# Kernel optimization log

Hardware: AMD Instinct MI355X
Metric: run time of the kernel (lower is better)

## Reference

```python
import jax, jax.numpy as jnp
import numpy as np

H = 64          # hidden_size / SINDy latent dim
DM = 128        # d_model (GRU input size)
FF = 128        # dim_feedforward
NL = 2          # num_sindy_layers
EPS = 1e-5      # LayerNorm eps (torch default)
TRI_I, TRI_J = np.triu_indices(H)          # poly_order=2 pairs, torch loop order (i<=j)
LIB = 1 + H + TRI_I.size                   # 2145


def layernorm(x, g, b):
    m = jnp.mean(x, axis=-1, keepdims=True)
    v = jnp.mean((x - m) ** 2, axis=-1, keepdims=True)
    return (x - m) * jax.lax.rsqrt(v + EPS) * g + b


def sindy_library(z):
    # z: (N, H) -> Theta: (N, 1 + H + H*(H+1)/2); same term ordering as torch loops
    ones = jnp.ones((z.shape[0], 1), z.dtype)
    quad = z[:, TRI_I] * z[:, TRI_J]
    return jnp.concatenate([ones, z, quad], axis=1)


def gru_layer(x, Wih, Whh, bih, bhh):
    # x: (B, S, in), Wih: (3H, in), Whh: (3H, H); torch GRU gate order r,z,n
    xp = jnp.einsum('bsi,gi->bsg', x, Wih) + bih  # (B,S,3H) precomputed input projections
    B = x.shape[0]

    def step(h, xpt):
        gh = h @ Whh.T + bhh
        r = jax.nn.sigmoid(xpt[:, :H] + gh[:, :H])
        z = jax.nn.sigmoid(xpt[:, H:2 * H] + gh[:, H:2 * H])
        n = jnp.tanh(xpt[:, 2 * H:] + r * gh[:, 2 * H:])
        h = (1.0 - z) * n + z * h
        return h, h

    h0 = jnp.zeros((B, H), x.dtype)
    _, ys = jax.lax.scan(step, h0, jnp.swapaxes(xp, 0, 1))  # scan over time
    return jnp.swapaxes(ys, 0, 1)  # (B, S, H)


def sindy_layer(src, coef, g1, b1n, W1, bf1, W2, bf2, g2, b2n):
    B, S, _ = src.shape
    theta = sindy_library(src.reshape(-1, H))          # (N, LIB)
    upd = (theta @ coef).reshape(B, S, H)              # (B, S, H)
    src = layernorm(src + upd, g1, b1n)                # dropout = identity (eval)
    ff = jax.nn.gelu(src @ W1.T + bf1, approximate=False) @ W2.T + bf2
    return layernorm(src + ff, g2, b2n)


def setup_inputs() -> dict:
    key = jax.random.key(0)
    ks = jax.random.split(key, 24)
    f = lambda k, sh, s=0.05: (jax.random.normal(k, sh, dtype=jnp.float32) * s)
    inp = {
        'x': jax.random.normal(ks[0], (32, 500, DM), dtype=jnp.float32),
        # GRU layer 0 (input DM) and layer 1 (input H)
        'Wih0': f(ks[1], (3 * H, DM)), 'Whh0': f(ks[2], (3 * H, H)),
        'bih0': f(ks[3], (3 * H,)), 'bhh0': f(ks[4], (3 * H,)),
        'Wih1': f(ks[5], (3 * H, H)), 'Whh1': f(ks[6], (3 * H, H)),
        'bih1': f(ks[7], (3 * H,)), 'bhh1': f(ks[8], (3 * H,)),
        # stacked params for NL=2 identical SINDy layers
        'coeffs': f(ks[9], (NL, LIB, H), 0.02),
        'ln1_g': jnp.ones((NL, H), jnp.float32), 'ln1_b': jnp.zeros((NL, H), jnp.float32),
        'W1': f(ks[10], (NL, FF, H)), 'b1': f(ks[11], (NL, FF)),
        'W2': f(ks[12], (NL, H, FF)), 'b2': f(ks[13], (NL, H)),
        'ln2_g': jnp.ones((NL, H), jnp.float32), 'ln2_b': jnp.zeros((NL, H), jnp.float32),
    }
    return inp


def reference(x, Wih0, Whh0, bih0, bhh0, Wih1, Whh1, bih1, bhh1,
              coeffs, ln1_g, ln1_b, W1, b1, W2, b2, ln2_g, ln2_b):
    h = gru_layer(x, Wih0, Whh0, bih0, bhh0)
    h = gru_layer(h, Wih1, Whh1, bih1, bhh1)
    for l in range(NL):
        h = sindy_layer(h, coeffs[l], ln1_g[l], ln1_b[l], W1[l], b1[l],
                        W2[l], b2[l], ln2_g[l], ln2_b[l])
    return h, h[:, -1, :]
```

## Files before the change

kernel.cpp:

```cpp
#include <hip/hip_runtime.h>
#include <hip/hip_bf16.h>
#include <math.h>

#define H 64
#define DM 128
#define GDIM 192
#define BSZ 32
#define SEQ 500
#define NROW (BSZ*SEQ)
#define LIBN 2145
#define FFD 128
#define KPAD 2176
#define NKC 68

typedef __attribute__((ext_vector_type(8))) short short8;
typedef __attribute__((ext_vector_type(4))) float f32x4;
typedef __attribute__((ext_vector_type(4))) unsigned u32x4;

__device__ __forceinline__ float sigf(float x) {
    return 1.0f / (1.0f + __expf(-x));
}
__device__ __forceinline__ float tanhfast(float x) {
    x = fminf(fmaxf(x, -15.0f), 15.0f);
    float t = __expf(-2.0f * x);
    return (1.0f - t) / (1.0f + t);
}
__device__ __forceinline__ short bf16r(float f) {
    unsigned u = __float_as_uint(f);
    unsigned r = (u + 0x7fffu + ((u >> 16) & 1u)) >> 16;
    return (short)r;
}

__global__ void pack_wih0(const float* __restrict__ w, float* __restrict__ wt) {
    int idx = blockIdx.x * 256 + threadIdx.x;
    if (idx >= GDIM * DM) return;
    int e  = idx & 3;
    int g  = (idx >> 2) % GDIM;
    int k4 = idx / (GDIM * 4);
    wt[idx] = w[g * DM + k4 * 4 + e];
}

__global__ void pack_coef_frag(const float* __restrict__ coef, short* __restrict__ cp) {
    int idx = blockIdx.x * 256 + threadIdx.x;
    int j = idx & 7, lane = (idx >> 3) & 63, nt = (idx >> 9) & 3, kc = idx >> 11;
    int k = kc * 32 + ((lane >> 4) << 3) + j;
    int c = nt * 16 + (lane & 15);
    float v = (k < LIBN) ? coef[(size_t)k * H + c] : 0.0f;
    cp[idx] = bf16r(v);
}
__global__ void pack_w1_frag(const float* __restrict__ w1, short* __restrict__ wp) {
    int idx = blockIdx.x * 256 + threadIdx.x;
    int j = idx & 7, lane = (idx >> 3) & 63, nt = (idx >> 9) & 7, kc = idx >> 12;
    int k = kc * 32 + ((lane >> 4) << 3) + j;
    int n = nt * 16 + (lane & 15);
    wp[idx] = bf16r(w1[(size_t)n * H + k]);
}
__global__ void pack_w2_frag(const float* __restrict__ w2, short* __restrict__ wp) {
    int idx = blockIdx.x * 256 + threadIdx.x;
    int j = idx & 7, lane = (idx >> 3) & 63, nt = (idx >> 9) & 3, kc = idx >> 11;
    int k = kc * 32 + ((lane >> 4) << 3) + j;
    int n = nt * 16 + (lane & 15);
    wp[idx] = bf16r(w2[(size_t)n * FFD + k]);
}

__global__ __launch_bounds__(192, 2) void xp0_gemm(const float* __restrict__ x,
                                                   const float* __restrict__ wtp,
                                                   const float* __restrict__ bih0,
                                                   float* __restrict__ xpT) {
    __shared__ float xs[64][DM];
    int rb = blockIdx.x * 64;
    for (int idx = threadIdx.x; idx < 64 * 32; idx += 192) {
        int r = idx >> 5, k4 = idx & 31;
        ((f32x4*)xs[r])[k4] = ((const f32x4*)(x + (size_t)(rb + r) * DM))[k4];
    }
    __syncthreads();
    int g = threadIdx.x;
    float bias = bih0[g];
    float acc[64];
#pragma unroll
    for (int r = 0; r < 64; r++) acc[r] = bias;
    for (int k4 = 0; k4 < 32; k4++) {
        f32x4 w4 = ((const f32x4*)wtp)[k4 * GDIM + g];
#pragma unroll
        for (int r = 0; r < 64; r++) {
            f32x4 xv = ((f32x4*)xs[r])[k4];
            acc[r] += w4[0] * xv[0] + w4[1] * xv[1] + w4[2] * xv[2] + w4[3] * xv[3];
        }
    }
    for (int r = 0; r < 64; r++) {
        int row = rb + r;
        int bb = row / 500;
        int ss = row - bb * 500;
        xpT[(((size_t)bb * 125 + (ss >> 2)) * GDIM + g) * 4 + (ss & 3)] = acc[r];
    }
}

__global__ __launch_bounds__(768, 3) void gru_fused(const float* __restrict__ xpT,
                                                    const float* __restrict__ whh0,
                                                    const float* __restrict__ bhh0,
                                                    const float* __restrict__ wih1,
                                                    const float* __restrict__ bih1,
                                                    const float* __restrict__ whh1,
                                                    const float* __restrict__ bhh1,
                                                    float* __restrict__ hbuf) {
    int b = blockIdx.x;
    int tid = threadIdx.x;
    int wv = __builtin_amdgcn_readfirstlane(tid >> 6);
    int lane = tid & 63;
    int m = wv % 3;
    int q = wv / 3;
    int k0 = q * 16;

    __shared__ __align__(16) float h0s[H];
    __shared__ __align__(16) float h1s[H];
    __shared__ float part[3][4][GDIM];

    if (tid < H) { h0s[tid] = 0.0f; h1s[tid] = 0.0f; }

    const float* W = (m == 0) ? whh0 : (m == 1) ? wih1 : whh1;
    float wr[16], wz[16], wn[16];
#pragma unroll
    for (int k4 = 0; k4 < 4; k4++) {
        f32x4 a = ((const f32x4*)(W + (size_t)lane * H + k0))[k4];
        f32x4 c = ((const f32x4*)(W + (size_t)(H + lane) * H + k0))[k4];
        f32x4 d = ((const f32x4*)(W + (size_t)(2 * H + lane) * H + k0))[k4];
        wr[4*k4] = a[0]; wr[4*k4+1] = a[1]; wr[4*k4+2] = a[2]; wr[4*k4+3] = a[3];
        wz[4*k4] = c[0]; wz[4*k4+1] = c[1]; wz[4*k4+2] = c[2]; wz[4*k4+3] = c[3];
        wn[4*k4] = d[0]; wn[4*k4+1] = d[1]; wn[4*k4+2] = d[2]; wn[4*k4+3] = d[3];
    }

    float b0r = 0, b0z = 0, b0n = 0;
    float b1ir = 0, b1iz = 0, b1in = 0, b1hr = 0, b1hz = 0, b1hn = 0;
    float hreg0 = 0.0f, hreg1 = 0.0f;
    float hb4[4] = {0.f, 0.f, 0.f, 0.f};
    f32x4 xc[4][3];
    const float* xpB = xpT + (size_t)b * 125 * GDIM * 4;

    if (wv == 0) {
        b0r = bhh0[lane]; b0z = bhh0[H + lane]; b0n = bhh0[2 * H + lane];
#pragma unroll
        for (int g3 = 0; g3 < 3; g3++) {
            xc[0][g3] = *(const f32x4*)(xpB + ((size_t)0 * GDIM + g3 * 64 + lane) * 4);
            xc[1][g3] = *(const f32x4*)(xpB + ((size_t)1 * GDIM + g3 * 64 + lane) * 4);
        }
    } else if (wv == 2) {
        b1ir = bih1[lane]; b1iz = bih1[H + lane]; b1in = bih1[2 * H + lane];
        b1hr = bhh1[lane]; b1hz = bhh1[H + lane]; b1hn = bhh1[2 * H + lane];
    }
    __syncthreads();

    auto loadch = [&](int c, int buf) {
        if (c < 125) {
#pragma unroll
            for (int g3 = 0; g3 < 3; g3++)
                xc[buf][g3] = *(const f32x4*)(xpB + ((size_t)c * GDIM + g3 * 64 + lane) * 4);
        }
    };

    auto step = [&](int s, int e, float xr, float xz, float xn) {
        const float* hv = (m == 2) ? h1s : h0s;
        float ar = 0, az = 0, an = 0;
#pragma unroll
        for (int t4 = 0; t4 < 4; t4++) {
            f32x4 h4 = ((const f32x4*)(hv + k0))[t4];
            ar += wr[4*t4] * h4[0] + wr[4*t4+1] * h4[1] + wr[4*t4+2] * h4[2] + wr[4*t4+3] * h4[3];
            az += wz[4*t4] * h4[0] + wz[4*t4+1] * h4[1] + wz[4*t4+2] * h4[2] + wz[4*t4+3] * h4[3];
            an += wn[4*t4] * h4[0] + wn[4*t4+1] * h4[1] + wn[4*t4+2] * h4[2] + wn[4*t4+3] * h4[3];
        }
        part[m][q][lane] = ar;
        part[m][q][H + lane] = az;
        part[m][q][2 * H + lane] = an;
        __syncthreads();

        if (wv == 0) {
            if (s < SEQ) {
                float gr = b0r, gz = b0z, gn = b0n;
#pragma unroll
                for (int qq = 0; qq < 4; qq++) {
                    gr += part[0][qq][lane];
                    gz += part[0][qq][H + lane];
                    gn += part[0][qq][2 * H + lane];
                }
                float rg = sigf(xr + gr);
                float zg = sigf(xz + gz);
                float ng = tanhfast(xn + rg * gn);
                hreg0 = (1.0f - zg) * ng + zg * hreg0;
                h0s[lane] = hreg0;
            }
        } else if (wv == 2) {
            if (s >= 1) {
                float xr1 = b1ir, xz1 = b1iz, xn1 = b1in;
                float gr1 = b1hr, gz1 = b1hz, gn1 = b1hn;
#pragma unroll
                for (int qq = 0; qq < 4; qq++) {
                    xr1 += part[1][qq][lane];
                    xz1 += part[1][qq][H + lane];
                    xn1 += part[1][qq][2 * H + lane];
                    gr1 += part[2][qq][lane];
                    gz1 += part[2][qq][H + lane];
                    gn1 += part[2][qq][2 * H + lane];
                }
                float rg = sigf(xr1 + gr1);
                float zg = sigf(xz1 + gz1);
                float ng = tanhfast(xn1 + rg * gn1);
                hreg1 = (1.0f - zg) * ng + zg * hreg1;
                h1s[lane] = hreg1;
                hb4[(e + 3) & 3] = hreg1;
                if (e == 0) {
                    float* dst = hbuf + ((size_t)b * SEQ + (s - 4)) * H + lane;
#pragma unroll
                    for (int t = 0; t < 4; t++) dst[t * H] = hb4[t];
                }
            }
        }
        __syncthreads();
    };

    for (int scb = 0; scb < 31; scb++) {
#pragma unroll
        for (int sci = 0; sci < 4; sci++) {
            int sc = scb * 4 + sci;
            if (wv == 0 && (sci & 1) == 0) {
                loadch(sc + 2, (sci + 2) & 3);
                loadch(sc + 3, (sci + 3) & 3);
            }
            int s0 = sc * 4;
            step(s0 + 0, 0, xc[sci][0][0], xc[sci][1][0], xc[sci][2][0]);
            step(s0 + 1, 1, xc[sci][0][1], xc[sci][1][1], xc[sci][2][1]);
            step(s0 + 2, 2, xc[sci][0][2], xc[sci][1][2], xc[sci][2][2]);
            step(s0 + 3, 3, xc[sci][0][3], xc[sci][1][3], xc[sci][2][3]);
        }
    }
    {
        step(496, 0, xc[0][0][0], xc[0][1][0], xc[0][2][0]);
        step(497, 1, xc[0][0][1], xc[0][1][1], xc[0][2][1]);
        step(498, 2, xc[0][0][2], xc[0][1][2], xc[0][2][2]);
        step(499, 3, xc[0][0][3], xc[0][1][3], xc[0][2][3]);
    }
    step(500, 0, 0.0f, 0.0f, 0.0f);
}

__global__ __launch_bounds__(512) void sindy_mfma(float* __restrict__ hbuf,
                                                  const short* __restrict__ cpk,
                                                  const short* __restrict__ w1p,
                                                  const short* __restrict__ w2p,
                                                  const float* __restrict__ g1,
                                                  const float* __restrict__ b1n,
                                                  const float* __restrict__ bf1,
                                                  const float* __restrict__ bf2v,
                                                  const float* __restrict__ g2,
                                                  const float* __restrict__ b2n,
                                                  float* __restrict__ out,
                                                  int final_layer) {
    __shared__ float z[64 * 68];
    __shared__ float upd[64 * 68];
    __shared__ float ff[64 * 132];
    __shared__ unsigned kmap[KPAD];
    __shared__ float bfs1[FFD], bfs2[H], g1s[H], b1s[H], g2s[H], b2s[H];

    int tid = threadIdx.x;
    int wv = __builtin_amdgcn_readfirstlane(tid >> 6);
    int lane = tid & 63;
    int row0 = blockIdx.x * 64;

    for (int idx = tid; idx < 64 * 16; idx += 512) {
        int r = idx >> 4, c4 = idx & 15;
        *(f32x4*)&z[r * 68 + c4 * 4] = *(const f32x4*)&hbuf[(size_t)(row0 + r) * H + c4 * 4];
    }
    for (int idx = tid; idx < 64 * 17; idx += 512)
        *(f32x4*)&upd[idx * 4] = (f32x4){0.f, 0.f, 0.f, 0.f};
    if (tid < 64) {
        z[tid * 68 + 64] = 1.0f; z[tid * 68 + 65] = 0.0f;
        z[tid * 68 + 66] = 0.0f; z[tid * 68 + 67] = 0.0f;
    }
    for (int k = tid; k < KPAD; k += 512) {
        unsigned a, b;
        if (k == 0) { a = 64; b = 64; }
        else if (k < 1 + H) { a = (unsigned)(k - 1); b = 64; }
        else if (k < LIBN) {
            int qq = k - (1 + H);
            double s = sqrt(16641.0 - 8.0 * (double)qq);
            int i = (int)((129.0 - s) * 0.5);
            int base = 64 * i - (i * (i - 1)) / 2;
            a = (unsigned)i; b = (unsigned)(i + (qq - base));
        } else { a = 65; b = 65; }
        kmap[k] = (a << 16) | b;
    }
    if (tid < FFD) bfs1[tid] = bf1[tid];
    if (tid < H) {
        bfs2[tid] = bf2v[tid];
        g1s[tid] = g1[tid]; b1s[tid] = b1n[tid];
        g2s[tid] = g2[tid]; b2s[tid] = b2n[tid];
    }
    __syncthreads();

    int kj0 = ((lane >> 4) << 3);
    int m0 = (wv & 3) * 16;
    int m = m0 + (lane & 15);
    int rbase = m0 + ((lane >> 4) << 2);
    int cb16 = lane & 15;
    const float* zrow = &z[m * 68];

    {
        int p = wv >> 2;
        f32x4 acc[4] = {{0,0,0,0},{0,0,0,0},{0,0,0,0},{0,0,0,0}};
        for (int kc = p; kc < NKC; kc += 2) {
            int kbase = kc * 32 + kj0;
            u32x4 km0 = *(const u32x4*)&kmap[kbase];
            u32x4 km1 = *(const u32x4*)&kmap[kbase + 4];
            short8 af;
            af[0] = bf16r(zrow[km0[0] >> 16] * zrow[km0[0] & 0xffff]);
            af[1] = bf16r(zrow[km0[1] >> 16] * zrow[km0[1] & 0xffff]);
            af[2] = bf16r(zrow[km0[2] >> 16] * zrow[km0[2] & 0xffff]);
            af[3] = bf16r(zrow[km0[3] >> 16] * zrow[km0[3] & 0xffff]);
            af[4] = bf16r(zrow[km1[0] >> 16] * zrow[km1[0] & 0xffff]);
            af[5] = bf16r(zrow[km1[1] >> 16] * zrow[km1[1] & 0xffff]);
            af[6] = bf16r(zrow[km1[2] >> 16] * zrow[km1[2] & 0xffff]);
            af[7] = bf16r(zrow[km1[3] >> 16] * zrow[km1[3] & 0xffff]);
            const short* cb = cpk + ((size_t)(kc * 4) * 64 + lane) * 8;
#pragma unroll
            for (int nt = 0; nt < 4; nt++) {
                short8 bf = *(const short8*)(cb + (size_t)nt * 512);
                acc[nt] = __builtin_amdgcn_mfma_f32_16x16x32_bf16(af, bf, acc[nt], 0, 0, 0);
            }
        }
#pragma unroll
        for (int nt = 0; nt < 4; nt++)
#pragma unroll
            for (int r = 0; r < 4; r++)
                atomicAdd(&upd[(rbase + r) * 68 + nt * 16 + cb16], acc[nt][r]);
    }
    __syncthreads();

    if (wv == 0) {
        float v[64];
        float s1 = 0.0f;
#pragma unroll
        for (int c = 0; c < 64; c++) { v[c] = z[lane * 68 + c] + upd[lane * 68 + c]; s1 += v[c]; }
        float mn = s1 * (1.0f / 64.0f);
        float s2 = 0.0f;
#pragma unroll
        for (int c = 0; c < 64; c++) { float d = v[c] - mn; s2 += d * d; }
        float rstd = 1.0f / sqrtf(s2 * (1.0f / 64.0f) + 1e-5f);
#pragma unroll
        for (int c = 0; c < 64; c++)
            z[lane * 68 + c] = (v[c] - mn) * rstd * g1s[c] + b1s[c];
    }
    __syncthreads();

    {
        int nq = wv >> 2;
        f32x4 acc[4] = {{0,0,0,0},{0,0,0,0},{0,0,0,0},{0,0,0,0}};
#pragma unroll
        for (int kc = 0; kc < 2; kc++) {
            f32x4 za = *(const f32x4*)&z[m * 68 + kc * 32 + kj0];
            f32x4 zb = *(const f32x4*)&z[m * 68 + kc * 32 + kj0 + 4];
            short8 af;
            af[0] = bf16r(za[0]); af[1] = bf16r(za[1]); af[2] = bf16r(za[2]); af[3] = bf16r(za[3]);
            af[4] = bf16r(zb[0]); af[5] = bf16r(zb[1]); af[6] = bf16r(zb[2]); af[7] = bf16r(zb[3]);
#pragma unroll
            for (int t = 0; t < 4; t++) {
                int nt = nq * 4 + t;
                short8 bf = *(const short8*)(w1p + ((size_t)(kc * 8 + nt) * 64 + lane) * 8);
                acc[t] = __builtin_amdgcn_mfma_f32_16x16x32_bf16(af, bf, acc[t], 0, 0, 0);
            }
        }
#pragma unroll
        for (int t = 0; t < 4; t++) {
            int col = (nq * 4 + t) * 16 + cb16;
#pragma unroll
            for (int r = 0; r < 4; r++) {
                float v = acc[t][r] + bfs1[col];
                ff[(rbase + r) * 132 + col] = 0.5f * v * (1.0f + erff(v * 0.70710678118654752f));
            }
        }
    }
    __syncthreads();

    {
        int nh = wv >> 2;
        f32x4 acc[2] = {{0,0,0,0},{0,0,0,0}};
        const float* frow = &ff[m * 132];
#pragma unroll
        for (int kc = 0; kc < 4; kc++) {
            f32x4 fa = *(const f32x4*)&frow[kc * 32 + kj0];
            f32x4 fb = *(const f32x4*)&frow[kc * 32 + kj0 + 4];
            short8 af;
            af[0] = bf16r(fa[0]); af[1] = bf16r(fa[1]); af[2] = bf16r(fa[2]); af[3] = bf16r(fa[3]);
            af[4] = bf16r(fb[0]); af[5] = bf16r(fb[1]); af[6] = bf16r(fb[2]); af[7] = bf16r(fb[3]);
#pragma unroll
            for (int t = 0; t < 2; t++) {
                int nt = nh * 2 + t;
                short8 bf = *(const short8*)(w2p + ((size_t)(kc * 4 + nt) * 64 + lane) * 8);
                acc[t] = __builtin_amdgcn_mfma_f32_16x16x32_bf16(af, bf, acc[t], 0, 0, 0);
            }
        }
#pragma unroll
        for (int t = 0; t < 2; t++) {
            int col = (nh * 2 + t) * 16 + cb16;
#pragma unroll
            for (int r = 0; r < 4; r++)
                upd[(rbase + r) * 68 + col] = acc[t][r] + bfs2[col];
        }
    }
    __syncthreads();

    if (wv == 0) {
        float v[64];
        float s1 = 0.0f;
#pragma unroll
        for (int c = 0; c < 64; c++) { v[c] = z[lane * 68 + c] + upd[lane * 68 + c]; s1 += v[c]; }
        float mn = s1 * (1.0f / 64.0f);
        float s2 = 0.0f;
#pragma unroll
        for (int c = 0; c < 64; c++) { float d = v[c] - mn; s2 += d * d; }
        float rstd = 1.0f / sqrtf(s2 * (1.0f / 64.0f) + 1e-5f);
        int row = row0 + lane;
#pragma unroll
        for (int c = 0; c < 64; c++) {
            float res = (v[c] - mn) * rstd * g2s[c] + b2s[c];
            if (!final_layer) {
                hbuf[(size_t)row * H + c] = res;
            } else {
                out[(size_t)row * H + c] = res;
                if (row % SEQ == SEQ - 1)
                    out[(size_t)NROW * H + (row / SEQ) * H + c] = res;
            }
        }
    }
}

extern "C" void kernel_launch(void* const* d_in, const int* in_sizes, int n_in,
                              void* d_out, int out_size, void* d_ws, size_t ws_size,
                              hipStream_t stream) {
    const float* x    = (const float*)d_in[0];
    const float* wih0 = (const float*)d_in[1];
    const float* whh0 = (const float*)d_in[2];
    const float* bih0 = (const float*)d_in[3];
    const float* bhh0 = (const float*)d_in[4];
    const float* wih1 = (const float*)d_in[5];
    const float* whh1 = (const float*)d_in[6];
    const float* bih1 = (const float*)d_in[7];
    const float* bhh1 = (const float*)d_in[8];
    const float* coeffs = (const float*)d_in[9];
    const float* ln1g = (const float*)d_in[10];
    const float* ln1b = (const float*)d_in[11];
    const float* w1   = (const float*)d_in[12];
    const float* b1   = (const float*)d_in[13];
    const float* w2   = (const float*)d_in[14];
    const float* b2   = (const float*)d_in[15];
    const float* ln2g = (const float*)d_in[16];
    const float* ln2b = (const float*)d_in[17];

    float* out = (float*)d_out;
    float* ws  = (float*)d_ws;
    float* xpT = ws;
    float* wtp = ws + (size_t)NROW * GDIM;
    short* bfa = (short*)(wtp + GDIM * DM);
    short* cpk[2] = { bfa, bfa + 139264 };
    short* w1pk[2] = { bfa + 2 * 139264, bfa + 2 * 139264 + 8192 };
    short* w2pk[2] = { bfa + 2 * 139264 + 2 * 8192, bfa + 2 * 139264 + 3 * 8192 };
    float* hbuf = out;

    pack_wih0<<<(GDIM * DM + 255) / 256, 256, 0, stream>>>(wih0, wtp);
    for (int l = 0; l < 2; l++) {
        pack_coef_frag<<<139264 / 256, 256, 0, stream>>>(coeffs + (size_t)l * LIBN * H, cpk[l]);
        pack_w1_frag<<<8192 / 256, 256, 0, stream>>>(w1 + (size_t)l * FFD * H, w1pk[l]);
        pack_w2_frag<<<8192 / 256, 256, 0, stream>>>(w2 + (size_t)l * H * FFD, w2pk[l]);
    }
    xp0_gemm<<<NROW / 64, 192, 0, stream>>>(x, wtp, bih0, xpT);
    gru_fused<<<BSZ, 768, 0, stream>>>(xpT, whh0, bhh0, wih1, bih1, whh1, bhh1, hbuf);
    for (int l = 0; l < 2; l++) {
        sindy_mfma<<<NROW / 64, 512, 0, stream>>>(
            hbuf, cpk[l], w1pk[l], w2pk[l],
            ln1g + l * H, ln1b + l * H, b1 + l * FFD,
            b2 + l * H, ln2g + l * H, ln2b + l * H,
            out, l == 1);
    }
}
```

Before: 554.9 us.

## Restructure GRU kernel to three waves with full-row register weights and one barrier per step

The fused two-layer GRU kernel drops from 12 waves with K-split partial sums reduced through shared memory to 3 waves. Each wave holds a full 192x64 weight slice in registers: wave 0 runs the layer-0 recurrence, wave 1 the layer-1 input projection, wave 2 the layer-1 recurrence. The stages are software-pipelined one step apart, with double-buffered shared state and a single lightweight barrier (lgkmcnt wait plus s_barrier) per step instead of two __syncthreads. This targets the per-step reduction and synchronisation latency on the serial critical path, at the cost of heavy register pressure (192 weight floats per lane), possible spills, and more serial FMA work per lane.

```diff
diff --git a/kernel.cpp b/kernel.cpp
--- a/kernel.cpp
+++ b/kernel.cpp
@@ -31,6 +31,8 @@
     return (short)r;
 }
 
+#define BAR_LGKM() asm volatile("s_waitcnt lgkmcnt(0)\n\ts_barrier" ::: "memory")
+
 __global__ void pack_wih0(const float* __restrict__ w, float* __restrict__ wt) {
     int idx = blockIdx.x * 256 + threadIdx.x;
     if (idx >= GDIM * DM) return;
@@ -95,7 +97,7 @@
     }
 }
 
-__global__ __launch_bounds__(768, 3) void gru_fused(const float* __restrict__ xpT,
+__global__ __launch_bounds__(192, 1) void gru_fused(const float* __restrict__ xpT,
                                                     const float* __restrict__ whh0,
                                                     const float* __restrict__ bhh0,
                                                     const float* __restrict__ wih1,
@@ -107,45 +109,35 @@
     int tid = threadIdx.x;
     int wv = __builtin_amdgcn_readfirstlane(tid >> 6);
     int lane = tid & 63;
-    int m = wv % 3;
-    int q = wv / 3;
-    int k0 = q * 16;
-
-    __shared__ __align__(16) float h0s[H];
-    __shared__ __align__(16) float h1s[H];
-    __shared__ float part[3][4][GDIM];
-
-    if (tid < H) { h0s[tid] = 0.0f; h1s[tid] = 0.0f; }
-
-    const float* W = (m == 0) ? whh0 : (m == 1) ? wih1 : whh1;
-    float wr[16], wz[16], wn[16];
-#pragma unroll
-    for (int k4 = 0; k4 < 4; k4++) {
-        f32x4 a = ((const f32x4*)(W + (size_t)lane * H + k0))[k4];
-        f32x4 c = ((const f32x4*)(W + (size_t)(H + lane) * H + k0))[k4];
-        f32x4 d = ((const f32x4*)(W + (size_t)(2 * H + lane) * H + k0))[k4];
-        wr[4*k4] = a[0]; wr[4*k4+1] = a[1]; wr[4*k4+2] = a[2]; wr[4*k4+3] = a[3];
-        wz[4*k4] = c[0]; wz[4*k4+1] = c[1]; wz[4*k4+2] = c[2]; wz[4*k4+3] = c[3];
-        wn[4*k4] = d[0]; wn[4*k4+1] = d[1]; wn[4*k4+2] = d[2]; wn[4*k4+3] = d[3];
-    }
-
-    float b0r = 0, b0z = 0, b0n = 0;
-    float b1ir = 0, b1iz = 0, b1in = 0, b1hr = 0, b1hz = 0, b1hn = 0;
+
+    __shared__ __align__(16) float h0s[2][H];
+    __shared__ __align__(16) float h1bc[H];
+    __shared__ __align__(16) float p1s[2][H][4];
+
+    if (tid < H) { h0s[1][tid] = 0.0f; h1bc[tid] = 0.0f; }
+
+    const float* W  = (wv == 0) ? whh0 : (wv == 1) ? wih1 : whh1;
+    const float* Bv = (wv == 0) ? bhh0 : (wv == 1) ? bih1 : bhh1;
+    f32x4 wrv[16], wzv[16], wnv[16];
+#pragma unroll
+    for (int t = 0; t < 16; t++) {
+        wrv[t] = ((const f32x4*)(W + (size_t)lane * H))[t];
+        wzv[t] = ((const f32x4*)(W + (size_t)(H + lane) * H))[t];
+        wnv[t] = ((const f32x4*)(W + (size_t)(2 * H + lane) * H))[t];
+    }
+    float br = Bv[lane], bz = Bv[H + lane], bn = Bv[2 * H + lane];
+
     float hreg0 = 0.0f, hreg1 = 0.0f;
     float hb4[4] = {0.f, 0.f, 0.f, 0.f};
     f32x4 xc[4][3];
     const float* xpB = xpT + (size_t)b * 125 * GDIM * 4;
 
     if (wv == 0) {
-        b0r = bhh0[lane]; b0z = bhh0[H + lane]; b0n = bhh0[2 * H + lane];
 #pragma unroll
         for (int g3 = 0; g3 < 3; g3++) {
             xc[0][g3] = *(const f32x4*)(xpB + ((size_t)0 * GDIM + g3 * 64 + lane) * 4);
             xc[1][g3] = *(const f32x4*)(xpB + ((size_t)1 * GDIM + g3 * 64 + lane) * 4);
         }
-    } else if (wv == 2) {
-        b1ir = bih1[lane]; b1iz = bih1[H + lane]; b1in = bih1[2 * H + lane];
-        b1hr = bhh1[lane]; b1hz = bhh1[H + lane]; b1hn = bhh1[2 * H + lane];
     }
     __syncthreads();
 
@@ -157,63 +149,59 @@
         }
     };
 
-    auto step = [&](int s, int e, float xr, float xz, float xn) {
-        const float* hv = (m == 2) ? h1s : h0s;
-        float ar = 0, az = 0, an = 0;
-#pragma unroll
-        for (int t4 = 0; t4 < 4; t4++) {
-            f32x4 h4 = ((const f32x4*)(hv + k0))[t4];
-            ar += wr[4*t4] * h4[0] + wr[4*t4+1] * h4[1] + wr[4*t4+2] * h4[2] + wr[4*t4+3] * h4[3];
-            az += wz[4*t4] * h4[0] + wz[4*t4+1] * h4[1] + wz[4*t4+2] * h4[2] + wz[4*t4+3] * h4[3];
-            an += wn[4*t4] * h4[0] + wn[4*t4+1] * h4[1] + wn[4*t4+2] * h4[2] + wn[4*t4+3] * h4[3];
-        }
-        part[m][q][lane] = ar;
-        part[m][q][H + lane] = az;
-        part[m][q][2 * H + lane] = an;
-        __syncthreads();
-
+    auto matvec = [&](const float* hb, float& gr, float& gz, float& gn) {
+        f32x4 hv[16];
+#pragma unroll
+        for (int t = 0; t < 16; t++) hv[t] = ((const f32x4*)hb)[t];
+        float ar = br, az = bz, an = bn;
+#pragma unroll
+        for (int t = 0; t < 16; t++) {
+            ar += wrv[t][0] * hv[t][0] + wrv[t][1] * hv[t][1]
+                + wrv[t][2] * hv[t][2] + wrv[t][3] * hv[t][3];
+            az += wzv[t][0] * hv[t][0] + wzv[t][1] * hv[t][1]
+                + wzv[t][2] * hv[t][2] + wzv[t][3] * hv[t][3];
+            an += wnv[t][0] * hv[t][0] + wnv[t][1] * hv[t][1]
+                + wnv[t][2] * hv[t][2] + wnv[t][3] * hv[t][3];
+        }
+        gr = ar; gz = az; gn = an;
+    };
+
+    auto step = [&](int u, int e, float xr, float xz, float xn) {
+        BAR_LGKM();
         if (wv == 0) {
-            if (s < SEQ) {
-                float gr = b0r, gz = b0z, gn = b0n;
-#pragma unroll
-                for (int qq = 0; qq < 4; qq++) {
-                    gr += part[0][qq][lane];
-                    gz += part[0][qq][H + lane];
-                    gn += part[0][qq][2 * H + lane];
-                }
+            if (u < SEQ) {
+                float gr, gz, gn;
+                matvec(h0s[(e + 1) & 1], gr, gz, gn);
                 float rg = sigf(xr + gr);
                 float zg = sigf(xz + gz);
                 float ng = tanhfast(xn + rg * gn);
                 hreg0 = (1.0f - zg) * ng + zg * hreg0;
-                h0s[lane] = hreg0;
-            }
-        } else if (wv == 2) {
-            if (s >= 1) {
-                float xr1 = b1ir, xz1 = b1iz, xn1 = b1in;
-                float gr1 = b1hr, gz1 = b1hz, gn1 = b1hn;
-#pragma unroll
-                for (int qq = 0; qq < 4; qq++) {
-                    xr1 += part[1][qq][lane];
-                    xz1 += part[1][qq][H + lane];
-                    xn1 += part[1][qq][2 * H + lane];
-                    gr1 += part[2][qq][lane];
-                    gz1 += part[2][qq][H + lane];
-                    gn1 += part[2][qq][2 * H + lane];
-                }
-                float rg = sigf(xr1 + gr1);
-                float zg = sigf(xz1 + gz1);
-                float ng = tanhfast(xn1 + rg * gn1);
+                h0s[e & 1][lane] = hreg0;
+            }
+        } else if (wv == 1) {
+            if (u >= 1 && u <= 500) {
+                float ar, az, an;
+                matvec(h0s[(e + 1) & 1], ar, az, an);
+                *(f32x4*)&p1s[(e + 1) & 1][lane][0] = (f32x4){ar, az, an, 0.0f};
+            }
+        } else {
+            if (u >= 2) {
+                float gr, gz, gn;
+                matvec(h1bc, gr, gz, gn);
+                f32x4 pv = *(const f32x4*)&p1s[e & 1][lane][0];
+                float rg = sigf(pv[0] + gr);
+                float zg = sigf(pv[1] + gz);
+                float ng = tanhfast(pv[2] + rg * gn);
                 hreg1 = (1.0f - zg) * ng + zg * hreg1;
-                h1s[lane] = hreg1;
-                hb4[(e + 3) & 3] = hreg1;
-                if (e == 0) {
-                    float* dst = hbuf + ((size_t)b * SEQ + (s - 4)) * H + lane;
+                h1bc[lane] = hreg1;
+                hb4[(e + 2) & 3] = hreg1;
+                if (e == 1) {
+                    float* dst = hbuf + ((size_t)b * SEQ + (u - 5)) * H + lane;
 #pragma unroll
                     for (int t = 0; t < 4; t++) dst[t * H] = hb4[t];
                 }
             }
         }
-        __syncthreads();
     };
 
     for (int scb = 0; scb < 31; scb++) {
@@ -238,6 +226,7 @@
         step(499, 3, xc[0][0][3], xc[0][1][3], xc[0][2][3]);
     }
     step(500, 0, 0.0f, 0.0f, 0.0f);
+    step(501, 1, 0.0f, 0.0f, 0.0f);
 }
 
 __global__ __launch_bounds__(512) void sindy_mfma(float* __restrict__ hbuf,
@@ -469,7 +458,7 @@
         pack_w2_frag<<<8192 / 256, 256, 0, stream>>>(w2 + (size_t)l * H * FFD, w2pk[l]);
     }
     xp0_gemm<<<NROW / 64, 192, 0, stream>>>(x, wtp, bih0, xpT);
-    gru_fused<<<BSZ, 768, 0, stream>>>(xpT, whh0, bhh0, wih1, bih1, whh1, bhh1, hbuf);
+    gru_fused<<<BSZ, 192, 0, stream>>>(xpT, whh0, bhh0, wih1, bih1, whh1, bhh1, hbuf);
     for (int l = 0; l < 2; l++) {
         sindy_mfma<<<NROW / 64, 512, 0, stream>>>(
             hbuf, cpk[l], w1pk[l], w2pk[l],
```

Result: slower. 679.1 us (+22.4%).

## Regroup SINDy library terms into 8-wide blocks sharing one multiplicand

Applied to the files above, without the earlier changes.

Reorders the quadratic library terms into groups of eight columns that share one factor z_a and use eight contiguous z_b values. The coefficient matrix is repacked to match, with zero rows where the group falls below the diagonal. This lets each lane build its MFMA A-fragment from one scalar and two vector LDS reads, replacing sixteen scattered reads. It also shrinks the per-block kmap setup, which used double sqrt. The cost is 75 K-chunks instead of 68, some of them padded with zeros.

```diff
diff --git a/kernel.cpp b/kernel.cpp
--- a/kernel.cpp
+++ b/kernel.cpp
@@ -10,8 +10,8 @@
 #define NROW (BSZ*SEQ)
 #define LIBN 2145
 #define FFD 128
-#define KPAD 2176
-#define NKC 68
+#define NKC2 75
+#define NGRP 300
 
 typedef __attribute__((ext_vector_type(8))) short short8;
 typedef __attribute__((ext_vector_type(4))) float f32x4;
@@ -29,6 +29,20 @@
     unsigned u = __float_as_uint(f);
     unsigned r = (u + 0x7fffu + ((u >> 16) & 1u)) >> 16;
     return (short)r;
+}
+
+__device__ __forceinline__ void grp_decode(int g, int& a, int& b) {
+    if (g < 8) { a = 64; b = g * 8; }
+    else if (g == 8 || g >= 297) { a = 64; b = 64; }
+    else {
+        int G = g - 9, acc = 0;
+        a = 0; b = 0;
+        for (int i2 = 0; i2 < 64; i2++) {
+            int cnt = 8 - (i2 >> 3);
+            if (G < acc + cnt) { a = i2; b = ((i2 >> 3) + (G - acc)) * 8; break; }
+            acc += cnt;
+        }
+    }
 }
 
 __global__ void pack_wih0(const float* __restrict__ w, float* __restrict__ wt) {
@@ -40,13 +54,21 @@
     wt[idx] = w[g * DM + k4 * 4 + e];
 }
 
-__global__ void pack_coef_frag(const float* __restrict__ coef, short* __restrict__ cp) {
+__global__ void pack_coef_frag2(const float* __restrict__ coef, short* __restrict__ cp) {
     int idx = blockIdx.x * 256 + threadIdx.x;
     int j = idx & 7, lane = (idx >> 3) & 63, nt = (idx >> 9) & 3, kc = idx >> 11;
-    int k = kc * 32 + ((lane >> 4) << 3) + j;
+    int grp = kc * 4 + (lane >> 4);
+    int row = -1;
+    if (grp < 8) row = 1 + grp * 8 + j;
+    else if (grp == 8) row = (j == 0) ? 0 : -1;
+    else if (grp < 297) {
+        int a, b;
+        grp_decode(grp, a, b);
+        int jdx = b + j;
+        if (jdx >= a) row = 65 + a * 64 - (a * (a - 1)) / 2 + (jdx - a);
+    }
     int c = nt * 16 + (lane & 15);
-    float v = (k < LIBN) ? coef[(size_t)k * H + c] : 0.0f;
-    cp[idx] = bf16r(v);
+    cp[idx] = (row >= 0) ? bf16r(coef[(size_t)row * H + c]) : (short)0;
 }
 __global__ void pack_w1_frag(const float* __restrict__ w1, short* __restrict__ wp) {
     int idx = blockIdx.x * 256 + threadIdx.x;
@@ -252,10 +274,10 @@
                                                   const float* __restrict__ b2n,
                                                   float* __restrict__ out,
                                                   int final_layer) {
-    __shared__ float z[64 * 68];
+    __shared__ float z[65 * 68];
     __shared__ float upd[64 * 68];
     __shared__ float ff[64 * 132];
-    __shared__ unsigned kmap[KPAD];
+    __shared__ unsigned kmap2[NGRP];
     __shared__ float bfs1[FFD], bfs2[H], g1s[H], b1s[H], g2s[H], b2s[H];
 
     int tid = threadIdx.x;
@@ -273,18 +295,11 @@
         z[tid * 68 + 64] = 1.0f; z[tid * 68 + 65] = 0.0f;
         z[tid * 68 + 66] = 0.0f; z[tid * 68 + 67] = 0.0f;
     }
-    for (int k = tid; k < KPAD; k += 512) {
-        unsigned a, b;
-        if (k == 0) { a = 64; b = 64; }
-        else if (k < 1 + H) { a = (unsigned)(k - 1); b = 64; }
-        else if (k < LIBN) {
-            int qq = k - (1 + H);
-            double s = sqrt(16641.0 - 8.0 * (double)qq);
-            int i = (int)((129.0 - s) * 0.5);
-            int base = 64 * i - (i * (i - 1)) / 2;
-            a = (unsigned)i; b = (unsigned)(i + (qq - base));
-        } else { a = 65; b = 65; }
-        kmap[k] = (a << 16) | b;
+    if (tid < 68) z[64 * 68 + tid] = 0.0f;
+    if (tid < NGRP) {
+        int a, b;
+        grp_decode(tid, a, b);
+        kmap2[tid] = ((unsigned)a << 16) | (unsigned)b;
     }
     if (tid < FFD) bfs1[tid] = bf1[tid];
     if (tid < H) {
@@ -304,19 +319,21 @@
     {
         int p = wv >> 2;
         f32x4 acc[4] = {{0,0,0,0},{0,0,0,0},{0,0,0,0},{0,0,0,0}};
-        for (int kc = p; kc < NKC; kc += 2) {
-            int kbase = kc * 32 + kj0;
-            u32x4 km0 = *(const u32x4*)&kmap[kbase];
-            u32x4 km1 = *(const u32x4*)&kmap[kbase + 4];
+        for (int kc = p; kc < NKC2; kc += 2) {
+            unsigned ab = kmap2[kc * 4 + (lane >> 4)];
+            float za = zrow[ab >> 16];
+            const float* zb = &zrow[ab & 0xffffu];
+            f32x4 z0 = *(const f32x4*)zb;
+            f32x4 z1 = *(const f32x4*)(zb + 4);
             short8 af;
-            af[0] = bf16r(zrow[km0[0] >> 16] * zrow[km0[0] & 0xffff]);
-            af[1] = bf16r(zrow[km0[1] >> 16] * zrow[km0[1] & 0xffff]);
-            af[2] = bf16r(zrow[km0[2] >> 16] * zrow[km0[2] & 0xffff]);
-            af[3] = bf16r(zrow[km0[3] >> 16] * zrow[km0[3] & 0xffff]);
-            af[4] = bf16r(zrow[km1[0] >> 16] * zrow[km1[0] & 0xffff]);
-            af[5] = bf16r(zrow[km1[1] >> 16] * zrow[km1[1] & 0xffff]);
-            af[6] = bf16r(zrow[km1[2] >> 16] * zrow[km1[2] & 0xffff]);
-            af[7] = bf16r(zrow[km1[3] >> 16] * zrow[km1[3] & 0xffff]);
+            af[0] = bf16r(za * z0[0]);
+            af[1] = bf16r(za * z0[1]);
+            af[2] = bf16r(za * z0[2]);
+            af[3] = bf16r(za * z0[3]);
+            af[4] = bf16r(za * z1[0]);
+            af[5] = bf16r(za * z1[1]);
+            af[6] = bf16r(za * z1[2]);
+            af[7] = bf16r(za * z1[3]);
             const short* cb = cpk + ((size_t)(kc * 4) * 64 + lane) * 8;
 #pragma unroll
             for (int nt = 0; nt < 4; nt++) {
@@ -457,14 +474,15 @@
     float* xpT = ws;
     float* wtp = ws + (size_t)NROW * GDIM;
     short* bfa = (short*)(wtp + GDIM * DM);
-    short* cpk[2] = { bfa, bfa + 139264 };
-    short* w1pk[2] = { bfa + 2 * 139264, bfa + 2 * 139264 + 8192 };
-    short* w2pk[2] = { bfa + 2 * 139264 + 2 * 8192, bfa + 2 * 139264 + 3 * 8192 };
+    const int CPK2 = NKC2 * 4 * 64 * 8;
+    short* cpk[2] = { bfa, bfa + CPK2 };
+    short* w1pk[2] = { bfa + 2 * CPK2, bfa + 2 * CPK2 + 8192 };
+    short* w2pk[2] = { bfa + 2 * CPK2 + 2 * 8192, bfa + 2 * CPK2 + 3 * 8192 };
     float* hbuf = out;
 
     pack_wih0<<<(GDIM * DM + 255) / 256, 256, 0, stream>>>(wih0, wtp);
     for (int l = 0; l < 2; l++) {
-        pack_coef_frag<<<139264 / 256, 256, 0, stream>>>(coeffs + (size_t)l * LIBN * H, cpk[l]);
+        pack_coef_frag2<<<CPK2 / 256, 256, 0, stream>>>(coeffs + (size_t)l * LIBN * H, cpk[l]);
         pack_w1_frag<<<8192 / 256, 256, 0, stream>>>(w1 + (size_t)l * FFD * H, w1pk[l]);
         pack_w2_frag<<<8192 / 256, 256, 0, stream>>>(w2 + (size_t)l * H * FFD, w2pk[l]);
     }
```

Measured after the change: 566.5 us. 2.1% more time.
